# Kernel tuning notes

Measured on AMD Instinct MI355X. Metric: run time of the kernel, lower is better.

The kernel has to match this reference:

```python
import jax, jax.numpy as jnp
import numpy as np

WS = (4, 4, 4)          # window size per axis
DISP = (2, 2, 2)        # cyclic-shift displacement = window_size // 2
HEADS = 8
HEAD_DIM = 32
DIM = 256


def _make_mask(x_shift, y_shift, z_shift):
    wx, wy, wz = WS
    dx, dy, dz = DISP
    m = np.zeros((wx, wy, wz, wx, wy, wz), np.float32)
    if x_shift:
        m[-dx:, :, :, :-dx, :, :] = -np.inf
        m[:-dx, :, :, -dx:, :, :] = -np.inf
    if y_shift:
        m[:, -dy:, :, :, :-dy, :] = -np.inf
        m[:, :-dy, :, :, -dy:, :] = -np.inf
    if z_shift:
        m[:, :, -dz:, :, :, :-dz] = -np.inf
        m[:, :, :-dz, :, :, -dz:] = -np.inf
    W = wx * wy * wz
    return jnp.asarray(m.reshape(W, W))


def setup_inputs() -> dict:
    key = jax.random.key(0)
    k1, k2, k3 = jax.random.split(key, 3)
    inner = HEADS * HEAD_DIM
    x = jax.random.normal(k1, (1, 48, 48, 48, DIM), jnp.float32)
    w_qkv = jax.random.normal(k2, (DIM, 3 * inner), jnp.float32) * (DIM ** -0.5)
    w_out = jax.random.normal(k3, (inner, DIM), jnp.float32) * (inner ** -0.5)
    b_out = jnp.zeros((DIM,), jnp.float32)
    return {"x": x, "w_qkv": w_qkv, "w_out": w_out, "b_out": b_out}


def reference(x, w_qkv, w_out, b_out):
    wx, wy, wz = WS
    h, d = HEADS, HEAD_DIM
    scale = d ** -0.5
    xm = _make_mask(True, False, False)
    ym = _make_mask(False, True, False)
    zm = _make_mask(False, False, True)

    # cyclic shift
    x = jnp.roll(x, (-DISP[0], -DISP[1], -DISP[2]), axis=(1, 2, 3))
    b, nx, ny, nz, _ = x.shape
    nwx, nwy, nwz = nx // wx, ny // wy, nz // wz
    W = wx * wy * wz
    nw = nwx * nwy * nwz

    qkv = x @ w_qkv                      # [b,nx,ny,nz,3*h*d]
    q, k, v = jnp.split(qkv, 3, axis=-1)

    def win(t):
        t = t.reshape(b, nwx, wx, nwy, wy, nwz, wz, h, d)
        t = t.transpose(0, 7, 1, 3, 5, 2, 4, 6, 8)   # b h nwx nwy nwz wx wy wz d
        return t.reshape(b, h, nw, W, d)

    q, k, v = win(q), win(k), win(v)
    dots = jnp.einsum('bhwid,bhwjd->bhwij', q, k) * scale

    # additive shift masks on the last window along each axis
    dots = dots.reshape(b, h, nwx, nwy, nwz, W, W)
    dots = dots.at[:, :, -1, :, :].add(xm)
    dots = dots.at[:, :, :, -1, :].add(ym)
    dots = dots.at[:, :, :, :, -1].add(zm)
    # faithful replication of original einops label mismatch: the tensor is
    # (nwx,nwy,nwz) but is flattened as if labeled (n_y,n_z,n_x) -> (n_x n_y n_z),
    # i.e. actual flatten order (nwz, nwx, nwy)
    dots = dots.transpose(0, 1, 4, 2, 3, 5, 6).reshape(b, h, nw, W, W)

    attn = jax.nn.softmax(dots, axis=-1)
    out = jnp.einsum('bhwij,bhwjd->bhwid', attn, v)

    out = out.reshape(b, h, nwx, nwy, nwz, wx, wy, wz, d)
    out = out.transpose(0, 2, 5, 3, 6, 4, 7, 1, 8).reshape(b, nx, ny, nz, h * d)
    out = out @ w_out + b_out
    # cyclic back shift
    return jnp.roll(out, DISP, axis=(1, 2, 3))
```

## Files before the change

### kernel.cpp

```cpp
#include <hip/hip_runtime.h>
#include <hip/hip_bf16.h>

typedef __attribute__((ext_vector_type(8))) short short8;
typedef __attribute__((ext_vector_type(4))) float f32x4;

#define NT 110592

static __device__ __forceinline__ unsigned int f2bf(float f){
  unsigned int x; __builtin_memcpy(&x,&f,4);
  x += 0x7fffu + ((x>>16)&1u);
  return x >> 16;
}

static __device__ __forceinline__ void gll16(const unsigned short* g, unsigned short* l){
  typedef const __attribute__((address_space(1))) unsigned int gu32;
  typedef __attribute__((address_space(3))) unsigned int lu32;
  __builtin_amdgcn_global_load_lds((gu32*)(const void*)g, (lu32*)(void*)l, 16, 0, 0);
}

__global__ void xconv(const float* __restrict__ x, unsigned short* __restrict__ o){
  size_t i = ((size_t)blockIdx.x*256 + threadIdx.x) * 8;
  float4 a = *(const float4*)(x+i), b = *(const float4*)(x+i+4);
  uint4 pk;
  pk.x = f2bf(a.x)|(f2bf(a.y)<<16); pk.y = f2bf(a.z)|(f2bf(a.w)<<16);
  pk.z = f2bf(b.x)|(f2bf(b.y)<<16); pk.w = f2bf(b.z)|(f2bf(b.w)<<16);
  *(uint4*)(o+i) = pk;
}

__global__ void tpose(const float* __restrict__ in, unsigned short* __restrict__ out,
                      int R, int Cc){
  int id = blockIdx.x*256 + threadIdx.x;
  if (id < R*Cc){ int r = id / Cc, c = id - r*Cc; out[c*R + r] = (unsigned short)f2bf(in[id]); }
}

template<bool CF32>
__global__ __launch_bounds__(512, 8) void gemm_bt(
    const unsigned short* __restrict__ A,
    const unsigned short* __restrict__ Bt,
    const float* __restrict__ bias,
    void* __restrict__ Cv,
    int M, int N, int K)
{
  __shared__ __align__(16) unsigned short As[2*4096];
  __shared__ __align__(16) unsigned short Bs[2*4096];

  const int nwg = gridDim.x;
  const int bid = blockIdx.x;
  const int qq = nwg >> 3, rr = nwg & 7;
  const int xcd = bid & 7, loc = bid >> 3;
  const int swz = (xcd < rr ? xcd*(qq+1) : rr*(qq+1) + (xcd-rr)*qq) + loc;
  const int nbn = N >> 7;
  const int bn = swz % nbn;
  const int bm = swz / nbn;

  const int tid  = threadIdx.x;
  const int lane = tid & 63;
  const int wave = tid >> 6;
  const int wm = wave >> 1, wn = wave & 1;
  const int l16 = lane & 15, q = lane >> 4;

  const size_t arow0 = (size_t)(bm*128 + (tid>>2))*K;
  const size_t brow0 = (size_t)(bn*128 + (tid>>2))*K;
  const int g8  = ((tid&3) ^ ((tid>>3)&3)) * 8;
  const int cg8 = (q ^ ((l16>>1)&3)) * 8;

  f32x4 acc[2][4] = {};

  for (int k0 = 0; k0 < K; k0 += 64){
    __syncthreads();
    gll16(A  + arow0 + k0 + g8,       &As[tid*8]);
    gll16(A  + arow0 + k0 + 32 + g8,  &As[4096 + tid*8]);
    gll16(Bt + brow0 + k0 + g8,       &Bs[tid*8]);
    gll16(Bt + brow0 + k0 + 32 + g8,  &Bs[4096 + tid*8]);
    __syncthreads();

    #pragma unroll
    for (int h = 0; h < 2; ++h){
      short8 af[2], bfm[4];
      #pragma unroll
      for (int t = 0; t < 2; ++t)
        af[t]  = *(const short8*)&As[h*4096 + (wm*32 + t*16 + l16)*32 + cg8];
      #pragma unroll
      for (int t = 0; t < 4; ++t)
        bfm[t] = *(const short8*)&Bs[h*4096 + (wn*64 + t*16 + l16)*32 + cg8];
      #pragma unroll
      for (int im = 0; im < 2; ++im)
        #pragma unroll
        for (int in = 0; in < 4; ++in)
          acc[im][in] = __builtin_amdgcn_mfma_f32_16x16x32_bf16(af[im], bfm[in], acc[im][in], 0, 0, 0);
    }
  }

  #pragma unroll
  for (int in = 0; in < 4; ++in){
    int col = bn*128 + wn*64 + in*16 + l16;
    float bv = CF32 ? bias[col] : 0.f;
    #pragma unroll
    for (int im = 0; im < 2; ++im){
      int row0 = bm*128 + wm*32 + im*16 + q*4;
      #pragma unroll
      for (int r = 0; r < 4; ++r){
        if (CF32) ((float*)Cv)[(size_t)(row0 + r)*N + col] = acc[im][in][r] + bv;
        else ((unsigned short*)Cv)[(size_t)(row0 + r)*N + col] = (unsigned short)f2bf(acc[im][in][r]);
      }
    }
  }
}

__global__ __launch_bounds__(256) void attn3d(
    const unsigned short* __restrict__ qkv,
    unsigned short* __restrict__ aout)
{
  __shared__ __align__(16) unsigned short sh[4*6912];
  const int tid  = threadIdx.x;
  const int wave = tid >> 6, lane = tid & 63;
  const int l16  = lane & 15, q = lane >> 4;
  unsigned short* P  = sh + wave*6912;
  unsigned short* VT = P + 64*72;

  const int wh   = blockIdx.x*4 + wave;
  const int head = wh & 7;
  const int w    = wh >> 3;
  const int A  = w / 144;
  const int B  = (w / 12) % 12;
  const int Cw = w % 12;

  const int iyy = l16 >> 2, izz = l16 & 3;
  int tok_qk[4], tok_v[4];
  #pragma unroll
  for (int t = 0; t < 4; ++t){
    int px = (4*B  + t   + 2) % 48;
    int py = (4*Cw + iyy + 2) % 48;
    int pz = (4*A  + izz + 2) % 48;
    tok_qk[t] = (px*48 + py)*48 + pz;
    int vx = (4*A  + t   + 2) % 48;
    int vy = (4*B  + iyy + 2) % 48;
    int vz = (4*Cw + izz + 2) % 48;
    tok_v[t] = (vx*48 + vy)*48 + vz;
  }

  {
    int sx = (4*A  + (lane>>4)     + 2) % 48;
    int sy = (4*B  + ((lane>>2)&3) + 2) % 48;
    int sz = (4*Cw + (lane&3)      + 2) % 48;
    const unsigned short* vp = qkv + (size_t)((sx*48+sy)*48+sz)*768 + 512 + head*32;
    uint4 v0 = *(const uint4*)(vp);
    uint4 v1 = *(const uint4*)(vp+8);
    uint4 v2 = *(const uint4*)(vp+16);
    uint4 v3 = *(const uint4*)(vp+24);
    unsigned vv[16] = {v0.x,v0.y,v0.z,v0.w, v1.x,v1.y,v1.z,v1.w,
                       v2.x,v2.y,v2.z,v2.w, v3.x,v3.y,v3.z,v3.w};
    #pragma unroll
    for (int u = 0; u < 16; ++u){
      VT[(2*u+0)*72 + lane] = (unsigned short)(vv[u] & 0xffffu);
      VT[(2*u+1)*72 + lane] = (unsigned short)(vv[u] >> 16);
    }
  }

  short8 kf[4], qf[4];
  #pragma unroll
  for (int t = 0; t < 4; ++t){
    const unsigned short* base = qkv + (size_t)tok_qk[t]*768 + head*32 + q*8;
    qf[t] = *(const short8*)(base);
    kf[t] = *(const short8*)(base + 256);
  }

  f32x4 s[4][4] = {};
  #pragma unroll
  for (int im = 0; im < 4; ++im)
    #pragma unroll
    for (int jn = 0; jn < 4; ++jn)
      s[im][jn] = __builtin_amdgcn_mfma_f32_16x16x32_bf16(kf[im], qf[jn], s[im][jn], 0, 0, 0);

  const float scale = 0.17677669529663687f;
  const int mx = (B == 11), my = (Cw == 11), mz = (A == 11);
  const int dy = my & ((q>>1) ^ (l16>>3));
  float sum4[4] = {0.f,0.f,0.f,0.f};
  #pragma unroll
  for (int jn = 0; jn < 4; ++jn){
    #pragma unroll
    for (int im = 0; im < 4; ++im){
      const int dxy = (mx & ((im>>1) ^ (jn>>1))) | dy;
      float e0 = (dxy | (mz & (0 ^ ((l16>>1)&1)))) ? 0.f : __expf(s[im][jn][0]*scale);
      float e1 = (dxy | (mz & (0 ^ ((l16>>1)&1)))) ? 0.f : __expf(s[im][jn][1]*scale);
      float e2 = (dxy | (mz & (1 ^ ((l16>>1)&1)))) ? 0.f : __expf(s[im][jn][2]*scale);
      float e3 = (dxy | (mz & (1 ^ ((l16>>1)&1)))) ? 0.f : __expf(s[im][jn][3]*scale);
      sum4[jn] += (e0+e1)+(e2+e3);
      uint2 pk;
      pk.x = f2bf(e0) | (f2bf(e1)<<16);
      pk.y = f2bf(e2) | (f2bf(e3)<<16);
      *(uint2*)&P[(jn*16+l16)*72 + im*16 + q*4] = pk;
    }
  }
  #pragma unroll
  for (int jn = 0; jn < 4; ++jn){
    float sj = sum4[jn];
    sj += __shfl_xor(sj, 16);
    sj += __shfl_xor(sj, 32);
    sum4[jn] = 1.f / sj;
  }

  f32x4 o[2][4] = {};
  #pragma unroll
  for (int ks = 0; ks < 2; ++ks){
    short8 vf[2], pf[4];
    #pragma unroll
    for (int dt = 0; dt < 2; ++dt)
      vf[dt] = *(const short8*)&VT[(dt*16 + l16)*72 + ks*32 + q*8];
    #pragma unroll
    for (int it = 0; it < 4; ++it)
      pf[it] = *(const short8*)&P[(it*16 + l16)*72 + ks*32 + q*8];
    #pragma unroll
    for (int dt = 0; dt < 2; ++dt)
      #pragma unroll
      for (int it = 0; it < 4; ++it)
        o[dt][it] = __builtin_amdgcn_mfma_f32_16x16x32_bf16(vf[dt], pf[it], o[dt][it], 0, 0, 0);
  }

  #pragma unroll
  for (int it = 0; it < 4; ++it){
    float inv = sum4[it];
    unsigned short* op = aout + (size_t)tok_v[it]*256 + head*32;
    #pragma unroll
    for (int dt = 0; dt < 2; ++dt){
      uint2 pk;
      pk.x = f2bf(o[dt][it][0]*inv) | (f2bf(o[dt][it][1]*inv) << 16);
      pk.y = f2bf(o[dt][it][2]*inv) | (f2bf(o[dt][it][3]*inv) << 16);
      *(uint2*)(op + dt*16 + q*4) = pk;
    }
  }
}

extern "C" void kernel_launch(void* const* d_in, const int* in_sizes, int n_in,
                              void* d_out, int out_size, void* d_ws, size_t ws_size,
                              hipStream_t stream) {
  const float* x     = (const float*)d_in[0];
  const float* w_qkv = (const float*)d_in[1];
  const float* w_out = (const float*)d_in[2];
  const float* b_out = (const float*)d_in[3];
  float* out = (float*)d_out;

  unsigned short* qkv   = (unsigned short*)d_ws;
  unsigned short* xbf   = qkv   + (size_t)NT*768;
  unsigned short* aout  = xbf;
  unsigned short* wqkvT = xbf   + (size_t)NT*256;
  unsigned short* woutT = wqkvT + (size_t)768*256;

  xconv<<<dim3(NT*256/2048), dim3(256), 0, stream>>>(x, xbf);
  tpose<<<dim3((256*768 + 255)/256), dim3(256), 0, stream>>>(w_qkv, wqkvT, 256, 768);
  tpose<<<dim3((256*256 + 255)/256), dim3(256), 0, stream>>>(w_out, woutT, 256, 256);

  gemm_bt<false><<<dim3((768/128)*(NT/128)), dim3(512), 0, stream>>>(xbf, wqkvT, nullptr, qkv, NT, 768, 256);

  attn3d<<<dim3(13824/4), dim3(256), 0, stream>>>(qkv, aout);

  gemm_bt<true><<<dim3((256/128)*(NT/128)), dim3(512), 0, stream>>>(aout, woutT, b_out, out, NT, 256, 256);
}
```

Before: 359.1 us.

## Fuse prep kernels, shrink attention blocks to two waves, raise MFMA priority

Merges the x bf16 conversion and both weight transposes into one prep launch, which removes two kernel launches. The attention kernel now runs two waves per block instead of four, with half the shared memory, so blocks are smaller and more of them fit per CU. s_setprio is raised around the MFMA sections so those waves get issue priority. Block count doubles, and the priority hints may have no effect.

```diff
diff --git a/kernel.cpp b/kernel.cpp
--- a/kernel.cpp
+++ b/kernel.cpp
@@ -18,19 +18,26 @@
   __builtin_amdgcn_global_load_lds((gu32*)(const void*)g, (lu32*)(void*)l, 16, 0, 0);
 }
 
-__global__ void xconv(const float* __restrict__ x, unsigned short* __restrict__ o){
-  size_t i = ((size_t)blockIdx.x*256 + threadIdx.x) * 8;
-  float4 a = *(const float4*)(x+i), b = *(const float4*)(x+i+4);
-  uint4 pk;
-  pk.x = f2bf(a.x)|(f2bf(a.y)<<16); pk.y = f2bf(a.z)|(f2bf(a.w)<<16);
-  pk.z = f2bf(b.x)|(f2bf(b.y)<<16); pk.w = f2bf(b.z)|(f2bf(b.w)<<16);
-  *(uint4*)(o+i) = pk;
-}
-
-__global__ void tpose(const float* __restrict__ in, unsigned short* __restrict__ out,
-                      int R, int Cc){
-  int id = blockIdx.x*256 + threadIdx.x;
-  if (id < R*Cc){ int r = id / Cc, c = id - r*Cc; out[c*R + r] = (unsigned short)f2bf(in[id]); }
+__global__ void prep(const float* __restrict__ x,      unsigned short* __restrict__ xbf,
+                     const float* __restrict__ wqkv,   unsigned short* __restrict__ wqkvT,
+                     const float* __restrict__ wout,   unsigned short* __restrict__ woutT){
+  const int bid = blockIdx.x;
+  if (bid < 13824){
+    size_t i = ((size_t)bid*256 + threadIdx.x) * 8;
+    float4 a = *(const float4*)(x+i), b = *(const float4*)(x+i+4);
+    uint4 pk;
+    pk.x = f2bf(a.x)|(f2bf(a.y)<<16); pk.y = f2bf(a.z)|(f2bf(a.w)<<16);
+    pk.z = f2bf(b.x)|(f2bf(b.y)<<16); pk.w = f2bf(b.z)|(f2bf(b.w)<<16);
+    *(uint4*)(xbf+i) = pk;
+  } else if (bid < 14592){
+    int id = (bid-13824)*256 + threadIdx.x;
+    int r = id / 768, c = id - r*768;
+    wqkvT[c*256 + r] = (unsigned short)f2bf(wqkv[id]);
+  } else {
+    int id = (bid-14592)*256 + threadIdx.x;
+    int r = id >> 8, c = id & 255;
+    woutT[c*256 + r] = (unsigned short)f2bf(wout[id]);
+  }
 }
 
 template<bool CF32>
@@ -107,18 +114,18 @@
   }
 }
 
-__global__ __launch_bounds__(256) void attn3d(
+__global__ __launch_bounds__(128) void attn3d(
     const unsigned short* __restrict__ qkv,
     unsigned short* __restrict__ aout)
 {
-  __shared__ __align__(16) unsigned short sh[4*6912];
+  __shared__ __align__(16) unsigned short sh[2*6912];
   const int tid  = threadIdx.x;
   const int wave = tid >> 6, lane = tid & 63;
   const int l16  = lane & 15, q = lane >> 4;
   unsigned short* P  = sh + wave*6912;
   unsigned short* VT = P + 64*72;
 
-  const int wh   = blockIdx.x*4 + wave;
+  const int wh   = blockIdx.x*2 + wave;
   const int head = wh & 7;
   const int w    = wh >> 3;
   const int A  = w / 144;
@@ -166,11 +173,13 @@
   }
 
   f32x4 s[4][4] = {};
+  __builtin_amdgcn_s_setprio(1);
   #pragma unroll
   for (int im = 0; im < 4; ++im)
     #pragma unroll
     for (int jn = 0; jn < 4; ++jn)
       s[im][jn] = __builtin_amdgcn_mfma_f32_16x16x32_bf16(kf[im], qf[jn], s[im][jn], 0, 0, 0);
+  __builtin_amdgcn_s_setprio(0);
 
   const float scale = 0.17677669529663687f;
   const int mx = (B == 11), my = (Cw == 11), mz = (A == 11);
@@ -201,6 +210,7 @@
   }
 
   f32x4 o[2][4] = {};
+  __builtin_amdgcn_s_setprio(1);
   #pragma unroll
   for (int ks = 0; ks < 2; ++ks){
     short8 vf[2], pf[4];
@@ -216,6 +226,7 @@
       for (int it = 0; it < 4; ++it)
         o[dt][it] = __builtin_amdgcn_mfma_f32_16x16x32_bf16(vf[dt], pf[it], o[dt][it], 0, 0, 0);
   }
+  __builtin_amdgcn_s_setprio(0);
 
   #pragma unroll
   for (int it = 0; it < 4; ++it){
@@ -246,13 +257,11 @@
   unsigned short* wqkvT = xbf   + (size_t)NT*256;
   unsigned short* woutT = wqkvT + (size_t)768*256;
 
-  xconv<<<dim3(NT*256/2048), dim3(256), 0, stream>>>(x, xbf);
-  tpose<<<dim3((256*768 + 255)/256), dim3(256), 0, stream>>>(w_qkv, wqkvT, 256, 768);
-  tpose<<<dim3((256*256 + 255)/256), dim3(256), 0, stream>>>(w_out, woutT, 256, 256);
+  prep<<<dim3(14848), dim3(256), 0, stream>>>(x, xbf, w_qkv, wqkvT, w_out, woutT);
 
   gemm_bt<false><<<dim3((768/128)*(NT/128)), dim3(512), 0, stream>>>(xbf, wqkvT, nullptr, qkv, NT, 768, 256);
 
-  attn3d<<<dim3(13824/4), dim3(256), 0, stream>>>(qkv, aout);
+  attn3d<<<dim3(13824/2), dim3(128), 0, stream>>>(qkv, aout);
 
   gemm_bt<true><<<dim3((256/128)*(NT/128)), dim3(512), 0, stream>>>(aout, woutT, b_out, out, NT, 256, 256);
 }
```

After: 339.4 us. -5.5%, faster.
